# Kernel optimization log

Measured on AMD Instinct MI355X. Metric: run time of the kernel, lower is better.

The kernel has to match this reference:

```python
import jax, jax.numpy as jnp
import numpy as np

DIM = 384
HEADS = 6
EPS = 1e-5
SCALE = DIM ** -0.5  # note: original uses full dim, not head_dim


def _dwconv_bn(x, w, stride, g, b, m, v):
    # x: [B, C, H, W], w: [C, 1, 3, 3] depthwise
    y = jax.lax.conv_general_dilated(
        x, w, window_strides=(stride, stride), padding=((1, 1), (1, 1)),
        dimension_numbers=('NCHW', 'OIHW', 'NCHW'), feature_group_count=DIM)
    # BatchNorm2d inference form
    inv = jax.lax.rsqrt(v + EPS)
    y = (y - m[None, :, None, None]) * (inv * g)[None, :, None, None] + b[None, :, None, None]
    # b c h w -> b (h w) c
    B, C, H, W = y.shape
    return y.reshape(B, C, H * W).transpose(0, 2, 1)


def setup_inputs() -> dict:
    key = jax.random.key(0)
    ks = jax.random.split(key, 24)
    d = {}
    d['x'] = jax.random.normal(ks[0], (8, 3136, DIM), jnp.float32)
    d['h'] = 56
    d['w'] = 56
    i = 1
    for nm in ('q', 'k', 'v'):
        d[f'conv_{nm}'] = jax.random.normal(ks[i], (DIM, 1, 3, 3), jnp.float32) * 0.1; i += 1
        d[f'bn{nm}_s'] = jnp.ones((DIM,), jnp.float32)
        d[f'bn{nm}_b'] = jnp.zeros((DIM,), jnp.float32)
        d[f'bn{nm}_m'] = jax.random.normal(ks[i], (DIM,), jnp.float32) * 0.1; i += 1
        d[f'bn{nm}_v'] = jax.random.uniform(ks[i], (DIM,), jnp.float32) + 0.5; i += 1
    s = DIM ** -0.5
    d['wq'] = jax.random.normal(ks[i], (DIM, DIM), jnp.float32) * s; i += 1
    d['wk'] = jax.random.normal(ks[i], (DIM, DIM), jnp.float32) * s; i += 1
    d['wv'] = jax.random.normal(ks[i], (DIM, DIM), jnp.float32) * s; i += 1
    d['w_last'] = jax.random.normal(ks[i], (DIM, DIM), jnp.float32) * s; i += 1
    d['b_last'] = jnp.zeros((DIM,), jnp.float32)
    return d


def reference(x, h, w, conv_q, bnq_s, bnq_b, bnq_m, bnq_v,
              conv_k, bnk_s, bnk_b, bnk_m, bnk_v,
              conv_v, bnv_s, bnv_b, bnv_m, bnv_v,
              wq, wk, wv, w_last, b_last):
    B, T, C = x.shape
    xim = x.transpose(0, 2, 1).reshape(B, C, h, w)  # b (h w) c -> b c h w
    q = _dwconv_bn(xim, conv_q, 1, bnq_s, bnq_b, bnq_m, bnq_v)  # [B, h*w, C]
    k = _dwconv_bn(xim, conv_k, 2, bnk_s, bnk_b, bnk_m, bnk_v)  # [B, hw/4, C]
    v = _dwconv_bn(xim, conv_v, 2, bnv_s, bnv_b, bnv_m, bnv_v)
    # linear projections (torch Linear: y = x @ W.T), split heads
    def heads(t, W):
        y = jnp.einsum('btc,oc->bto', t, W)
        Bt, Tt, _ = y.shape
        return y.reshape(Bt, Tt, HEADS, C // HEADS).transpose(0, 2, 1, 3)
    qh, kh, vh = heads(q, wq), heads(k, wk), heads(v, wv)
    attn = jax.nn.softmax(jnp.einsum('bhld,bhtd->bhlt', qh, kh) * SCALE, axis=-1)
    o = jnp.einsum('bhlt,bhtd->bhld', attn, vh)  # [B, H, L, d]
    o = o.transpose(0, 2, 1, 3).reshape(B, T, C)
    return jnp.einsum('btc,oc->bto', o, w_last) + b_last
```

## Files before the change

kernel.cpp:

```cpp
#include <hip/hip_runtime.h>
#include <hip/hip_bf16.h>

typedef __bf16 bf16;
typedef __attribute__((ext_vector_type(8))) __bf16 bf16x8;
typedef __attribute__((ext_vector_type(4))) __bf16 bf16x4;
typedef __attribute__((ext_vector_type(4))) float floatx4;

#define MFMA16(a, b, c) __builtin_amdgcn_mfma_f32_16x16x32_bf16((a), (b), (c), 0, 0, 0)

#define DIM 384
#define T1 3136
#define T2 784
#define T2P 832
#define B_ 8
#define EPSV 1e-5f

__device__ __forceinline__ void gload_lds16(const bf16* g, bf16* l) {
  __builtin_amdgcn_global_load_lds(
      (const __attribute__((address_space(1))) void*)g,
      (__attribute__((address_space(3))) void*)l, 16, 0, 0);
}

__global__ void conv_q_kernel(const float* __restrict__ x,
                              const float* __restrict__ wc,
                              const float* __restrict__ g, const float* __restrict__ bb,
                              const float* __restrict__ mm, const float* __restrict__ vv,
                              bf16* __restrict__ out) {
  int blk = blockIdx.x;
  int c = threadIdx.x;
  int xg = blk % 14;
  int y = (blk / 14) % 56;
  int b = blk / (14 * 56);
  int x0 = xg * 4;
  const float* xb = x + (size_t)b * T1 * DIM;
  float wr[9];
#pragma unroll
  for (int i = 0; i < 9; ++i) wr[i] = wc[c * 9 + i];
  float a = rsqrtf(vv[c] + EPSV) * g[c];
  float bia = bb[c] - mm[c] * a;
  float in[3][6];
#pragma unroll
  for (int r = 0; r < 3; ++r) {
    int yy = y + r - 1;
#pragma unroll
    for (int cc = 0; cc < 6; ++cc) {
      int xc = x0 + cc - 1;
      in[r][cc] = (yy >= 0 && yy < 56 && xc >= 0 && xc < 56)
                      ? xb[(yy * 56 + xc) * DIM + c] : 0.f;
    }
  }
#pragma unroll
  for (int p = 0; p < 4; ++p) {
    float s = 0.f;
#pragma unroll
    for (int r = 0; r < 3; ++r)
#pragma unroll
      for (int dx = 0; dx < 3; ++dx) s += in[r][p + dx] * wr[r * 3 + dx];
    out[((size_t)b * T1 + y * 56 + x0 + p) * DIM + c] = (bf16)(s * a + bia);
  }
}

__global__ void conv_kv_kernel(const float* __restrict__ x,
    const float* __restrict__ wkc, const float* __restrict__ gk, const float* __restrict__ bk,
    const float* __restrict__ mk, const float* __restrict__ vk,
    const float* __restrict__ wvc, const float* __restrict__ gv, const float* __restrict__ bv,
    const float* __restrict__ mv, const float* __restrict__ vvv,
    bf16* __restrict__ kout, bf16* __restrict__ vout) {
  int blk = blockIdx.x;
  int c = threadIdx.x;
  int xg = blk % 7;
  int y2 = (blk / 7) % 28;
  int b = blk / (7 * 28);
  int x20 = xg * 4;
  const float* xb = x + (size_t)b * T1 * DIM;
  float wk9[9], wv9[9];
#pragma unroll
  for (int i = 0; i < 9; ++i) { wk9[i] = wkc[c * 9 + i]; wv9[i] = wvc[c * 9 + i]; }
  float ak = rsqrtf(vk[c] + EPSV) * gk[c];
  float av = rsqrtf(vvv[c] + EPSV) * gv[c];
  float bik = bk[c] - mk[c] * ak;
  float biv = bv[c] - mv[c] * av;
  float in[3][9];
  int y = 2 * y2;
#pragma unroll
  for (int r = 0; r < 3; ++r) {
    int yy = y + r - 1;
#pragma unroll
    for (int cc = 0; cc < 9; ++cc) {
      int xc = 2 * x20 + cc - 1;
      in[r][cc] = (yy >= 0 && yy < 56 && xc >= 0 && xc < 56)
                      ? xb[(yy * 56 + xc) * DIM + c] : 0.f;
    }
  }
#pragma unroll
  for (int p = 0; p < 4; ++p) {
    float sk = 0.f, sv = 0.f;
#pragma unroll
    for (int r = 0; r < 3; ++r)
#pragma unroll
      for (int dx = 0; dx < 3; ++dx) {
        float xv = in[r][2 * p + dx];
        sk += xv * wk9[r * 3 + dx];
        sv += xv * wv9[r * 3 + dx];
      }
    size_t o = ((size_t)b * T2 + y2 * 28 + x20 + p) * DIM + c;
    kout[o] = (bf16)(sk * ak + bik);
    vout[o] = (bf16)(sv * av + biv);
  }
}

__global__ void cvt4_kernel(const float* __restrict__ s0, const float* __restrict__ s1,
                            const float* __restrict__ s2, const float* __restrict__ s3,
                            bf16* __restrict__ d0, bf16* __restrict__ d1,
                            bf16* __restrict__ d2, bf16* __restrict__ d3) {
  int i = blockIdx.x * 256 + threadIdx.x;
  d0[i] = (bf16)s0[i];
  d1[i] = (bf16)s1[i];
  d2[i] = (bf16)s2[i];
  d3[i] = (bf16)s3[i];
}

#define BK 32
__global__ __launch_bounds__(256)
void gemm_bf16_kernel(const bf16* __restrict__ A, const bf16* __restrict__ Bw,
                      void* __restrict__ out, const float* __restrict__ bias,
                      int M, int mode, float scale) {
  __shared__ bf16 Al[128 * BK];
  __shared__ bf16 Bl[128 * BK];
  int tid = threadIdx.x;
  int m0 = blockIdx.x * 128, n0 = blockIdx.y * 128;
  int w = tid >> 6, lane = tid & 63;
  int wm = w >> 1, wn = w & 1;
  int l16 = lane & 15, quad = lane >> 4;
  floatx4 acc[4][4];
#pragma unroll
  for (int i = 0; i < 4; ++i)
#pragma unroll
    for (int j = 0; j < 4; ++j) acc[i][j] = (floatx4){0.f, 0.f, 0.f, 0.f};

  int srow = w * 32 + (lane >> 2);
  int scol = (lane & 3) * 8;
  const bf16* ag0 = &A[(size_t)(m0 + srow) * DIM + scol];
  const bf16* ag1 = ag0 + (size_t)16 * DIM;
  const bf16* bg0 = &Bw[(size_t)(n0 + srow) * DIM + scol];
  const bf16* bg1 = bg0 + (size_t)16 * DIM;
  bf16* la0 = &Al[(w * 32) * BK];
  bf16* la1 = &Al[(w * 32 + 16) * BK];
  bf16* lb0 = &Bl[(w * 32) * BK];
  bf16* lb1 = &Bl[(w * 32 + 16) * BK];

  for (int k0 = 0; k0 < DIM; k0 += BK) {
    __syncthreads();
    gload_lds16(ag0 + k0, la0);
    gload_lds16(ag1 + k0, la1);
    gload_lds16(bg0 + k0, lb0);
    gload_lds16(bg1 + k0, lb1);
    __syncthreads();
    bf16x8 af[4], bfr[4];
#pragma unroll
    for (int i = 0; i < 4; ++i) {
      af[i]  = *(const bf16x8*)&Al[(wm * 64 + i * 16 + l16) * BK + quad * 8];
      bfr[i] = *(const bf16x8*)&Bl[(wn * 64 + i * 16 + l16) * BK + quad * 8];
    }
#pragma unroll
    for (int i = 0; i < 4; ++i)
#pragma unroll
      for (int j = 0; j < 4; ++j)
        acc[i][j] = MFMA16(af[i], bfr[j], acc[i][j]);
  }
#pragma unroll
  for (int i = 0; i < 4; ++i) {
#pragma unroll
    for (int j = 0; j < 4; ++j) {
#pragma unroll
      for (int rr = 0; rr < 4; ++rr) {
        int row = m0 + wm * 64 + i * 16 + quad * 4 + rr;
        int col = n0 + wn * 64 + j * 16 + l16;
        float v = acc[i][j][rr];
        if (mode == 3) {
          ((float*)out)[(size_t)row * DIM + col] = v + bias[col];
        } else if (mode == 2) {
          int b = row / T2;
          int t = row - b * T2;
          ((bf16*)out)[((size_t)b * DIM + col) * T2P + t] = (bf16)v;
        } else {
          ((bf16*)out)[(size_t)row * DIM + col] = (bf16)(v * scale);
        }
      }
    }
  }
}

#define PLDS 72
__global__ __launch_bounds__(256, 4)
void attn_kernel(const bf16* __restrict__ Qp, const bf16* __restrict__ Kp,
                 const bf16* __restrict__ Vt, bf16* __restrict__ Ob) {
  __shared__ bf16 Kl[64 * 64];
  __shared__ bf16 Vl[64 * 64];
  __shared__ bf16 Pl[4][2][16 * PLDS];
  int blk = blockIdx.x;
  int qblk = blk % 25;
  int h = (blk / 25) % 6;
  int b = blk / (25 * 6);
  int tid = threadIdx.x, w = tid >> 6, lane = tid & 63;
  int l16 = lane & 15, quad = lane >> 4;
  int q0w = qblk * 128 + w * 32;

  bf16x8 qf[2][2];
#pragma unroll
  for (int qt = 0; qt < 2; ++qt) {
    int qi = q0w + qt * 16 + l16;
    qi = qi < T1 ? qi : T1 - 1;
    const bf16* qp = &Qp[((size_t)b * T1 + qi) * DIM + h * 64];
    qf[qt][0] = *(const bf16x8*)&qp[quad * 8];
    qf[qt][1] = *(const bf16x8*)&qp[32 + quad * 8];
  }
  floatx4 oacc[2][4];
#pragma unroll
  for (int qt = 0; qt < 2; ++qt)
#pragma unroll
    for (int dt = 0; dt < 4; ++dt) oacc[qt][dt] = (floatx4){0.f, 0.f, 0.f, 0.f};
  float lsum[2] = {0.f, 0.f};

  int rsub = lane >> 3;
  int chnk = (lane & 7) ^ rsub;
  const bf16* kg0 = &Kp[((size_t)b * T2 + w * 16 + rsub) * DIM + h * 64 + chnk * 8];
  const bf16* kg1 = kg0 + (size_t)8 * DIM;
  const bf16* vg0 = &Vt[((size_t)b * DIM + h * 64 + w * 16 + rsub) * T2P + chnk * 8];
  const bf16* vg1 = vg0 + (size_t)8 * T2P;
  bf16* kl0 = &Kl[(w * 16) * 64];
  bf16* kl1 = &Kl[(w * 16 + 8) * 64];
  bf16* vl0 = &Vl[(w * 16) * 64];
  bf16* vl1 = &Vl[(w * 16 + 8) * 64];

  int sw = l16 & 7;
  bf16* pw0 = &Pl[w][0][l16 * PLDS + quad * 4];
  bf16* pr0 = &Pl[w][0][l16 * PLDS + quad * 8];

  for (int it = 0; it < 12; ++it) {
    __syncthreads();
    gload_lds16(kg0, kl0);
    gload_lds16(kg1, kl1);
    gload_lds16(vg0, vl0);
    gload_lds16(vg1, vl1);
    __syncthreads();
#pragma unroll
    for (int mt = 0; mt < 4; ++mt) {
      int krow = (mt * 16 + l16) * 64;
      bf16x8 kf0 = *(const bf16x8*)&Kl[krow + ((quad) ^ sw) * 8];
      bf16x8 kf1 = *(const bf16x8*)&Kl[krow + ((quad + 4) ^ sw) * 8];
#pragma unroll
      for (int qt = 0; qt < 2; ++qt) {
        floatx4 z = (floatx4){0.f, 0.f, 0.f, 0.f};
        z = MFMA16(kf0, qf[qt][0], z);
        z = MFMA16(kf1, qf[qt][1], z);
        float p0 = __builtin_amdgcn_exp2f(z[0]);
        float p1 = __builtin_amdgcn_exp2f(z[1]);
        float p2 = __builtin_amdgcn_exp2f(z[2]);
        float p3 = __builtin_amdgcn_exp2f(z[3]);
        lsum[qt] += (p0 + p1) + (p2 + p3);
        bf16x4 pw = (bf16x4){(bf16)p0, (bf16)p1, (bf16)p2, (bf16)p3};
        *(bf16x4*)(pw0 + qt * 16 * PLDS + mt * 16) = pw;
      }
    }
#pragma unroll
    for (int kt = 0; kt < 2; ++kt) {
      bf16x8 pf0 = *(const bf16x8*)(pr0 + kt * 32);
      bf16x8 pf1 = *(const bf16x8*)(pr0 + 16 * PLDS + kt * 32);
#pragma unroll
      for (int dt = 0; dt < 4; ++dt) {
        bf16x8 vf = *(const bf16x8*)&Vl[(dt * 16 + l16) * 64 + ((kt * 4 + quad) ^ sw) * 8];
        oacc[0][dt] = MFMA16(vf, pf0, oacc[0][dt]);
        oacc[1][dt] = MFMA16(vf, pf1, oacc[1][dt]);
      }
    }
    kg0 += (size_t)64 * DIM; kg1 += (size_t)64 * DIM;
    vg0 += 64; vg1 += 64;
  }
  {
    const bf16* kptr = &Kp[((size_t)b * T2 + 768 + l16) * DIM + h * 64 + quad * 8];
    const bf16* vptr = &Vt[((size_t)b * DIM + h * 64 + l16) * T2P + 768 + quad * 8];
    bf16x8 kf0 = *(const bf16x8*)(kptr);
    bf16x8 kf1 = *(const bf16x8*)(kptr + 32);
    bf16x4 zz = (bf16x4){(bf16)0.f, (bf16)0.f, (bf16)0.f, (bf16)0.f};
#pragma unroll
    for (int qt = 0; qt < 2; ++qt) {
      floatx4 z = (floatx4){0.f, 0.f, 0.f, 0.f};
      z = MFMA16(kf0, qf[qt][0], z);
      z = MFMA16(kf1, qf[qt][1], z);
      float p0 = __builtin_amdgcn_exp2f(z[0]);
      float p1 = __builtin_amdgcn_exp2f(z[1]);
      float p2 = __builtin_amdgcn_exp2f(z[2]);
      float p3 = __builtin_amdgcn_exp2f(z[3]);
      lsum[qt] += (p0 + p1) + (p2 + p3);
      bf16x4 pw = (bf16x4){(bf16)p0, (bf16)p1, (bf16)p2, (bf16)p3};
      *(bf16x4*)(pw0 + qt * 16 * PLDS) = pw;
      *(bf16x4*)(pw0 + qt * 16 * PLDS + 16) = zz;
    }
    bf16x8 pf0 = *(const bf16x8*)(pr0);
    bf16x8 pf1 = *(const bf16x8*)(pr0 + 16 * PLDS);
#pragma unroll
    for (int dt = 0; dt < 4; ++dt) {
      bf16x8 vf = *(const bf16x8*)(vptr + (size_t)dt * 16 * T2P);
      oacc[0][dt] = MFMA16(vf, pf0, oacc[0][dt]);
      oacc[1][dt] = MFMA16(vf, pf1, oacc[1][dt]);
    }
  }
#pragma unroll
  for (int qt = 0; qt < 2; ++qt) {
    float l = lsum[qt];
    l += __shfl_xor(l, 16);
    l += __shfl_xor(l, 32);
    float inv = 1.f / l;
    int qg = q0w + qt * 16 + l16;
    if (qg < T1) {
      bf16* op = &Ob[((size_t)b * T1 + qg) * DIM + h * 64];
#pragma unroll
      for (int dt = 0; dt < 4; ++dt) {
        floatx4 o = oacc[qt][dt];
        bf16x4 ov = (bf16x4){(bf16)(o[0] * inv), (bf16)(o[1] * inv),
                             (bf16)(o[2] * inv), (bf16)(o[3] * inv)};
        *(bf16x4*)&op[dt * 16 + quad * 4] = ov;
      }
    }
  }
}

extern "C" void kernel_launch(void* const* d_in, const int* in_sizes, int n_in,
                              void* d_out, int out_size, void* d_ws, size_t ws_size,
                              hipStream_t stream) {
  (void)in_sizes; (void)n_in; (void)out_size; (void)ws_size;
  const float* x      = (const float*)d_in[0];
  const float* conv_q = (const float*)d_in[3];
  const float* bnq_s  = (const float*)d_in[4];
  const float* bnq_b  = (const float*)d_in[5];
  const float* bnq_m  = (const float*)d_in[6];
  const float* bnq_v  = (const float*)d_in[7];
  const float* conv_k = (const float*)d_in[8];
  const float* bnk_s  = (const float*)d_in[9];
  const float* bnk_b  = (const float*)d_in[10];
  const float* bnk_m  = (const float*)d_in[11];
  const float* bnk_v  = (const float*)d_in[12];
  const float* conv_v = (const float*)d_in[13];
  const float* bnv_s  = (const float*)d_in[14];
  const float* bnv_b  = (const float*)d_in[15];
  const float* bnv_m  = (const float*)d_in[16];
  const float* bnv_v  = (const float*)d_in[17];
  const float* wq     = (const float*)d_in[18];
  const float* wk     = (const float*)d_in[19];
  const float* wv     = (const float*)d_in[20];
  const float* wl     = (const float*)d_in[21];
  const float* b_last = (const float*)d_in[22];

  char* ws = (char*)d_ws;
  bf16* q_act = (bf16*)(ws + 0);
  bf16* k_act = (bf16*)(ws + 19267584);
  bf16* v_act = (bf16*)(ws + 24084480);
  bf16* Qp    = (bf16*)(ws + 28901376);
  bf16* Kp    = (bf16*)(ws + 48168960);
  bf16* Vtp   = (bf16*)(ws + 52985856);
  bf16* wqb   = (bf16*)(ws + 58097664);
  bf16* wkb   = wqb + 147456;
  bf16* wvb   = wkb + 147456;
  bf16* wlb   = wvb + 147456;

  const float QSCALE = 0.05103103630798288f * 1.4426950408889634f;

  conv_q_kernel<<<B_ * 56 * 14, DIM, 0, stream>>>(x, conv_q, bnq_s, bnq_b, bnq_m, bnq_v, q_act);
  conv_kv_kernel<<<B_ * 28 * 7, DIM, 0, stream>>>(x, conv_k, bnk_s, bnk_b, bnk_m, bnk_v,
                                                  conv_v, bnv_s, bnv_b, bnv_m, bnv_v,
                                                  k_act, v_act);
  cvt4_kernel<<<576, 256, 0, stream>>>(wq, wk, wv, wl, wqb, wkb, wvb, wlb);

  gemm_bf16_kernel<<<dim3(196, 3), 256, 0, stream>>>(q_act, wqb, Qp, nullptr,
                                                     B_ * T1, 1, QSCALE);
  gemm_bf16_kernel<<<dim3(49, 3), 256, 0, stream>>>(k_act, wkb, Kp, nullptr,
                                                    B_ * T2, 0, 1.f);
  gemm_bf16_kernel<<<dim3(49, 3), 256, 0, stream>>>(v_act, wvb, Vtp, nullptr,
                                                    B_ * T2, 2, 1.f);

  attn_kernel<<<25 * 6 * B_, 256, 0, stream>>>(Qp, Kp, Vtp, q_act);

  gemm_bf16_kernel<<<dim3(196, 3), 256, 0, stream>>>(q_act, wlb, d_out, b_last,
                                                     B_ * T1, 3, 1.f);
}
```

Before: 281.1 us.

## Fuse conv kernels and weight cast, merge QKV GEMMs, swizzle attention P buffer

Merges the q and k/v depthwise conv kernels and the weight bf16 cast into one kernel, so stride-2 k/v outputs are computed from the same loaded input window on even rows. The three QKV projection GEMMs become a single launch with blocks dispatched by index range. In attention, the padded P scratch is replaced by an XOR-swizzled 64-wide layout, which cuts LDS use and allows the occupancy hint to rise from 4 to 5 blocks. This removes several kernel launches and a redundant read of x, at the cost of load imbalance in the conv kernel, since odd rows skip the k/v work.

After: 283.5 us. No clear change (+0.9%).

```diff
diff --git a/kernel.cpp b/kernel.cpp
--- a/kernel.cpp
+++ b/kernel.cpp
@@ -21,23 +21,30 @@
       (__attribute__((address_space(3))) void*)l, 16, 0, 0);
 }
 
-__global__ void conv_q_kernel(const float* __restrict__ x,
-                              const float* __restrict__ wc,
-                              const float* __restrict__ g, const float* __restrict__ bb,
-                              const float* __restrict__ mm, const float* __restrict__ vv,
-                              bf16* __restrict__ out) {
+__global__ void conv_fused_kernel(const float* __restrict__ x,
+    const float* __restrict__ wqc, const float* __restrict__ gq, const float* __restrict__ bq,
+    const float* __restrict__ mq, const float* __restrict__ vq,
+    const float* __restrict__ wkc, const float* __restrict__ gk, const float* __restrict__ bk,
+    const float* __restrict__ mk, const float* __restrict__ vk,
+    const float* __restrict__ wvc, const float* __restrict__ gv, const float* __restrict__ bv,
+    const float* __restrict__ mv, const float* __restrict__ vvv,
+    bf16* __restrict__ qout, bf16* __restrict__ kout, bf16* __restrict__ vout,
+    const float* __restrict__ w0, const float* __restrict__ w1,
+    const float* __restrict__ w2, const float* __restrict__ w3,
+    bf16* __restrict__ d0, bf16* __restrict__ d1,
+    bf16* __restrict__ d2, bf16* __restrict__ d3) {
   int blk = blockIdx.x;
   int c = threadIdx.x;
+  int gid = blk * DIM + c;
+  if (gid < 147456) {
+    d0[gid] = (bf16)w0[gid]; d1[gid] = (bf16)w1[gid];
+    d2[gid] = (bf16)w2[gid]; d3[gid] = (bf16)w3[gid];
+  }
   int xg = blk % 14;
   int y = (blk / 14) % 56;
   int b = blk / (14 * 56);
   int x0 = xg * 4;
   const float* xb = x + (size_t)b * T1 * DIM;
-  float wr[9];
-#pragma unroll
-  for (int i = 0; i < 9; ++i) wr[i] = wc[c * 9 + i];
-  float a = rsqrtf(vv[c] + EPSV) * g[c];
-  float bia = bb[c] - mm[c] * a;
   float in[3][6];
 #pragma unroll
   for (int r = 0; r < 3; ++r) {
@@ -49,86 +56,54 @@
                       ? xb[(yy * 56 + xc) * DIM + c] : 0.f;
     }
   }
-#pragma unroll
-  for (int p = 0; p < 4; ++p) {
-    float s = 0.f;
-#pragma unroll
-    for (int r = 0; r < 3; ++r)
-#pragma unroll
-      for (int dx = 0; dx < 3; ++dx) s += in[r][p + dx] * wr[r * 3 + dx];
-    out[((size_t)b * T1 + y * 56 + x0 + p) * DIM + c] = (bf16)(s * a + bia);
-  }
-}
-
-__global__ void conv_kv_kernel(const float* __restrict__ x,
-    const float* __restrict__ wkc, const float* __restrict__ gk, const float* __restrict__ bk,
-    const float* __restrict__ mk, const float* __restrict__ vk,
-    const float* __restrict__ wvc, const float* __restrict__ gv, const float* __restrict__ bv,
-    const float* __restrict__ mv, const float* __restrict__ vvv,
-    bf16* __restrict__ kout, bf16* __restrict__ vout) {
-  int blk = blockIdx.x;
-  int c = threadIdx.x;
-  int xg = blk % 7;
-  int y2 = (blk / 7) % 28;
-  int b = blk / (7 * 28);
-  int x20 = xg * 4;
-  const float* xb = x + (size_t)b * T1 * DIM;
-  float wk9[9], wv9[9];
-#pragma unroll
-  for (int i = 0; i < 9; ++i) { wk9[i] = wkc[c * 9 + i]; wv9[i] = wvc[c * 9 + i]; }
-  float ak = rsqrtf(vk[c] + EPSV) * gk[c];
-  float av = rsqrtf(vvv[c] + EPSV) * gv[c];
-  float bik = bk[c] - mk[c] * ak;
-  float biv = bv[c] - mv[c] * av;
-  float in[3][9];
-  int y = 2 * y2;
-#pragma unroll
-  for (int r = 0; r < 3; ++r) {
-    int yy = y + r - 1;
-#pragma unroll
-    for (int cc = 0; cc < 9; ++cc) {
-      int xc = 2 * x20 + cc - 1;
-      in[r][cc] = (yy >= 0 && yy < 56 && xc >= 0 && xc < 56)
-                      ? xb[(yy * 56 + xc) * DIM + c] : 0.f;
-    }
-  }
-#pragma unroll
-  for (int p = 0; p < 4; ++p) {
-    float sk = 0.f, sv = 0.f;
-#pragma unroll
-    for (int r = 0; r < 3; ++r)
-#pragma unroll
-      for (int dx = 0; dx < 3; ++dx) {
-        float xv = in[r][2 * p + dx];
-        sk += xv * wk9[r * 3 + dx];
-        sv += xv * wv9[r * 3 + dx];
-      }
-    size_t o = ((size_t)b * T2 + y2 * 28 + x20 + p) * DIM + c;
-    kout[o] = (bf16)(sk * ak + bik);
-    vout[o] = (bf16)(sv * av + biv);
-  }
-}
-
-__global__ void cvt4_kernel(const float* __restrict__ s0, const float* __restrict__ s1,
-                            const float* __restrict__ s2, const float* __restrict__ s3,
-                            bf16* __restrict__ d0, bf16* __restrict__ d1,
-                            bf16* __restrict__ d2, bf16* __restrict__ d3) {
-  int i = blockIdx.x * 256 + threadIdx.x;
-  d0[i] = (bf16)s0[i];
-  d1[i] = (bf16)s1[i];
-  d2[i] = (bf16)s2[i];
-  d3[i] = (bf16)s3[i];
+  {
+    float wr[9];
+#pragma unroll
+    for (int i = 0; i < 9; ++i) wr[i] = wqc[c * 9 + i];
+    float a = rsqrtf(vq[c] + EPSV) * gq[c];
+    float bia = bq[c] - mq[c] * a;
+#pragma unroll
+    for (int p = 0; p < 4; ++p) {
+      float s = 0.f;
+#pragma unroll
+      for (int r = 0; r < 3; ++r)
+#pragma unroll
+        for (int dx = 0; dx < 3; ++dx) s += in[r][p + dx] * wr[r * 3 + dx];
+      qout[((size_t)b * T1 + y * 56 + x0 + p) * DIM + c] = (bf16)(s * a + bia);
+    }
+  }
+  if ((y & 1) == 0) {
+    int y2 = y >> 1;
+    float wk9[9], wv9[9];
+#pragma unroll
+    for (int i = 0; i < 9; ++i) { wk9[i] = wkc[c * 9 + i]; wv9[i] = wvc[c * 9 + i]; }
+    float ak = rsqrtf(vk[c] + EPSV) * gk[c];
+    float av = rsqrtf(vvv[c] + EPSV) * gv[c];
+    float bik = bk[c] - mk[c] * ak;
+    float biv = bv[c] - mv[c] * av;
+#pragma unroll
+    for (int p2 = 0; p2 < 2; ++p2) {
+      float sk = 0.f, sv = 0.f;
+#pragma unroll
+      for (int r = 0; r < 3; ++r)
+#pragma unroll
+        for (int dx = 0; dx < 3; ++dx) {
+          float xv = in[r][2 * p2 + dx];
+          sk += xv * wk9[r * 3 + dx];
+          sv += xv * wv9[r * 3 + dx];
+        }
+      size_t o = ((size_t)b * T2 + y2 * 28 + (x0 >> 1) + p2) * DIM + c;
+      kout[o] = (bf16)(sk * ak + bik);
+      vout[o] = (bf16)(sv * av + biv);
+    }
+  }
 }
 
 #define BK 32
-__global__ __launch_bounds__(256)
-void gemm_bf16_kernel(const bf16* __restrict__ A, const bf16* __restrict__ Bw,
-                      void* __restrict__ out, const float* __restrict__ bias,
-                      int M, int mode, float scale) {
-  __shared__ bf16 Al[128 * BK];
-  __shared__ bf16 Bl[128 * BK];
+__device__ __forceinline__
+void gemm_body(const bf16* A, const bf16* Bw, void* out, const float* bias,
+               int mode, float scale, int m0, int n0, bf16* Al, bf16* Bl) {
   int tid = threadIdx.x;
-  int m0 = blockIdx.x * 128, n0 = blockIdx.y * 128;
   int w = tid >> 6, lane = tid & 63;
   int wm = w >> 1, wn = w & 1;
   int l16 = lane & 15, quad = lane >> 4;
@@ -191,13 +166,34 @@
   }
 }
 
-#define PLDS 72
-__global__ __launch_bounds__(256, 4)
+__global__ __launch_bounds__(256)
+void qkv_gemm_kernel(const bf16* q_act, const bf16* k_act, const bf16* v_act,
+                     const bf16* wqb, const bf16* wkb, const bf16* wvb,
+                     bf16* Qp, bf16* Kp, bf16* Vtp, float qscale) {
+  __shared__ bf16 Al[128 * BK];
+  __shared__ bf16 Bl[128 * BK];
+  int bx = blockIdx.x;
+  const bf16 *A, *Bw; void* out; int mode, t; float scale;
+  if (bx < 588)      { A = q_act; Bw = wqb; out = Qp;  mode = 1; scale = qscale; t = bx; }
+  else if (bx < 735) { A = k_act; Bw = wkb; out = Kp;  mode = 0; scale = 1.f; t = bx - 588; }
+  else               { A = v_act; Bw = wvb; out = Vtp; mode = 2; scale = 1.f; t = bx - 735; }
+  gemm_body(A, Bw, out, nullptr, mode, scale, (t / 3) * 128, (t % 3) * 128, Al, Bl);
+}
+
+__global__ __launch_bounds__(256)
+void last_gemm_kernel(const bf16* A, const bf16* Bw, float* out, const float* bias) {
+  __shared__ bf16 Al[128 * BK];
+  __shared__ bf16 Bl[128 * BK];
+  int bx = blockIdx.x;
+  gemm_body(A, Bw, out, bias, 3, 1.f, (bx / 3) * 128, (bx % 3) * 128, Al, Bl);
+}
+
+__global__ __launch_bounds__(256, 5)
 void attn_kernel(const bf16* __restrict__ Qp, const bf16* __restrict__ Kp,
                  const bf16* __restrict__ Vt, bf16* __restrict__ Ob) {
   __shared__ bf16 Kl[64 * 64];
   __shared__ bf16 Vl[64 * 64];
-  __shared__ bf16 Pl[4][2][16 * PLDS];
+  __shared__ bf16 Pl[4][2][16 * 64];
   int blk = blockIdx.x;
   int qblk = blk % 25;
   int h = (blk / 25) % 6;
@@ -233,9 +229,7 @@
   bf16* vl0 = &Vl[(w * 16) * 64];
   bf16* vl1 = &Vl[(w * 16 + 8) * 64];
 
-  int sw = l16 & 7;
-  bf16* pw0 = &Pl[w][0][l16 * PLDS + quad * 4];
-  bf16* pr0 = &Pl[w][0][l16 * PLDS + quad * 8];
+  int key = l16 & 7;
 
   for (int it = 0; it < 12; ++it) {
     __syncthreads();
@@ -247,8 +241,9 @@
 #pragma unroll
     for (int mt = 0; mt < 4; ++mt) {
       int krow = (mt * 16 + l16) * 64;
-      bf16x8 kf0 = *(const bf16x8*)&Kl[krow + ((quad) ^ sw) * 8];
-      bf16x8 kf1 = *(const bf16x8*)&Kl[krow + ((quad + 4) ^ sw) * 8];
+      bf16x8 kf0 = *(const bf16x8*)&Kl[krow + ((quad) ^ key) * 8];
+      bf16x8 kf1 = *(const bf16x8*)&Kl[krow + ((quad + 4) ^ key) * 8];
+      int pchunk = (((mt * 2 + (quad >> 1)) ^ key) << 3) + (quad & 1) * 4;
 #pragma unroll
       for (int qt = 0; qt < 2; ++qt) {
         floatx4 z = (floatx4){0.f, 0.f, 0.f, 0.f};
@@ -260,16 +255,17 @@
         float p3 = __builtin_amdgcn_exp2f(z[3]);
         lsum[qt] += (p0 + p1) + (p2 + p3);
         bf16x4 pw = (bf16x4){(bf16)p0, (bf16)p1, (bf16)p2, (bf16)p3};
-        *(bf16x4*)(pw0 + qt * 16 * PLDS + mt * 16) = pw;
+        *(bf16x4*)&Pl[w][qt][l16 * 64 + pchunk] = pw;
       }
     }
 #pragma unroll
     for (int kt = 0; kt < 2; ++kt) {
-      bf16x8 pf0 = *(const bf16x8*)(pr0 + kt * 32);
-      bf16x8 pf1 = *(const bf16x8*)(pr0 + 16 * PLDS + kt * 32);
+      int rchunk = ((kt * 4 + quad) ^ key) << 3;
+      bf16x8 pf0 = *(const bf16x8*)&Pl[w][0][l16 * 64 + rchunk];
+      bf16x8 pf1 = *(const bf16x8*)&Pl[w][1][l16 * 64 + rchunk];
 #pragma unroll
       for (int dt = 0; dt < 4; ++dt) {
-        bf16x8 vf = *(const bf16x8*)&Vl[(dt * 16 + l16) * 64 + ((kt * 4 + quad) ^ sw) * 8];
+        bf16x8 vf = *(const bf16x8*)&Vl[(dt * 16 + l16) * 64 + ((kt * 4 + quad) ^ key) * 8];
         oacc[0][dt] = MFMA16(vf, pf0, oacc[0][dt]);
         oacc[1][dt] = MFMA16(vf, pf1, oacc[1][dt]);
       }
@@ -283,6 +279,8 @@
     bf16x8 kf0 = *(const bf16x8*)(kptr);
     bf16x8 kf1 = *(const bf16x8*)(kptr + 32);
     bf16x4 zz = (bf16x4){(bf16)0.f, (bf16)0.f, (bf16)0.f, (bf16)0.f};
+    int pc0 = ((((quad >> 1)) ^ key) << 3) + (quad & 1) * 4;
+    int pc1 = (((2 + (quad >> 1)) ^ key) << 3) + (quad & 1) * 4;
 #pragma unroll
     for (int qt = 0; qt < 2; ++qt) {
       floatx4 z = (floatx4){0.f, 0.f, 0.f, 0.f};
@@ -294,11 +292,12 @@
       float p3 = __builtin_amdgcn_exp2f(z[3]);
       lsum[qt] += (p0 + p1) + (p2 + p3);
       bf16x4 pw = (bf16x4){(bf16)p0, (bf16)p1, (bf16)p2, (bf16)p3};
-      *(bf16x4*)(pw0 + qt * 16 * PLDS) = pw;
-      *(bf16x4*)(pw0 + qt * 16 * PLDS + 16) = zz;
-    }
-    bf16x8 pf0 = *(const bf16x8*)(pr0);
-    bf16x8 pf1 = *(const bf16x8*)(pr0 + 16 * PLDS);
+      *(bf16x4*)&Pl[w][qt][l16 * 64 + pc0] = pw;
+      *(bf16x4*)&Pl[w][qt][l16 * 64 + pc1] = zz;
+    }
+    int rchunk = (quad ^ key) << 3;
+    bf16x8 pf0 = *(const bf16x8*)&Pl[w][0][l16 * 64 + rchunk];
+    bf16x8 pf1 = *(const bf16x8*)&Pl[w][1][l16 * 64 + rchunk];
 #pragma unroll
     for (int dt = 0; dt < 4; ++dt) {
       bf16x8 vf = *(const bf16x8*)(vptr + (size_t)dt * 16 * T2P);
@@ -366,21 +365,18 @@
 
   const float QSCALE = 0.05103103630798288f * 1.4426950408889634f;
 
-  conv_q_kernel<<<B_ * 56 * 14, DIM, 0, stream>>>(x, conv_q, bnq_s, bnq_b, bnq_m, bnq_v, q_act);
-  conv_kv_kernel<<<B_ * 28 * 7, DIM, 0, stream>>>(x, conv_k, bnk_s, bnk_b, bnk_m, bnk_v,
-                                                  conv_v, bnv_s, bnv_b, bnv_m, bnv_v,
-                                                  k_act, v_act);
-  cvt4_kernel<<<576, 256, 0, stream>>>(wq, wk, wv, wl, wqb, wkb, wvb, wlb);
-
-  gemm_bf16_kernel<<<dim3(196, 3), 256, 0, stream>>>(q_act, wqb, Qp, nullptr,
-                                                     B_ * T1, 1, QSCALE);
-  gemm_bf16_kernel<<<dim3(49, 3), 256, 0, stream>>>(k_act, wkb, Kp, nullptr,
-                                                    B_ * T2, 0, 1.f);
-  gemm_bf16_kernel<<<dim3(49, 3), 256, 0, stream>>>(v_act, wvb, Vtp, nullptr,
-                                                    B_ * T2, 2, 1.f);
+  conv_fused_kernel<<<B_ * 56 * 14, DIM, 0, stream>>>(
+      x,
+      conv_q, bnq_s, bnq_b, bnq_m, bnq_v,
+      conv_k, bnk_s, bnk_b, bnk_m, bnk_v,
+      conv_v, bnv_s, bnv_b, bnv_m, bnv_v,
+      q_act, k_act, v_act,
+      wq, wk, wv, wl, wqb, wkb, wvb, wlb);
+
+  qkv_gemm_kernel<<<882, 256, 0, stream>>>(q_act, k_act, v_act, wqb, wkb, wvb,
+                                           Qp, Kp, Vtp, QSCALE);
 
   attn_kernel<<<25 * 6 * B_, 256, 0, stream>>>(Qp, Kp, Vtp, q_act);
 
-  gemm_bf16_kernel<<<dim3(196, 3), 256, 0, stream>>>(q_act, wlb, d_out, b_last,
-                                                     B_ * T1, 3, 1.f);
-}
+  last_gemm_kernel<<<588, 256, 0, stream>>>(q_act, wlb, (float*)d_out, b_last);
+}
```
